# Optimization experiments

Hardware: AMD Instinct MI355X
Metric: run time of the kernel (lower is better)

Reference implementation:

```python
import jax, jax.numpy as jnp
import numpy as np
from jax import lax

B, T, K = 32, 2048, 1024


def setup_inputs() -> dict:
    key = jax.random.key(0)
    x = jax.random.normal(key, (B, T, K), dtype=jnp.float32)
    return {"x": x}


def reference(x) -> jnp.ndarray:
    # x: [B, T, K]. Max-plus DP:
    #   out[:, 0]   = x[:, 0]
    #   out[:, i+1] = x[:, i+1] + max(out[:, i], shift_right(out[:, i], -inf))
    neg_inf = jnp.asarray(-jnp.inf, dtype=x.dtype)
    x_t = jnp.swapaxes(x, 0, 1)  # [T, B, K] time-major for scan

    def step(carry, xi):
        # carry: [B, K] = out row i; xi: [B, K] = x row i+1
        shifted = jnp.concatenate(
            [jnp.full_like(carry[:, :1], neg_inf), carry[:, :-1]], axis=1
        )
        new = xi + jnp.maximum(carry, shifted)
        return new, new

    init = x_t[0]
    _, rows = lax.scan(step, init, x_t[1:])  # rows: [T-1, B, K]
    out = jnp.concatenate([init[None], rows], axis=0)  # [T, B, K]
    return jnp.swapaxes(out, 0, 1)  # [B, T, K]
```

## Files before the change

### kernel.cpp

```cpp
#include <hip/hip_runtime.h>
#include <math.h>


#define BB 32
#define TT 2048
#define KK 1024
#define GG 8
#define WW (KK / GG)
#define RR 32
#define NT (TT / RR)

typedef __attribute__((address_space(1))) void GV;
typedef __attribute__((address_space(3))) void LV;

__global__ __launch_bounds__(64, 1)
void harddtw_td(const float* __restrict__ x, float* __restrict__ out,
                int* __restrict__ flags, float* __restrict__ bws)
{
    const int bid  = blockIdx.x;
    const int g    = bid >> 5;
    const int b    = bid & 31;
    const int lane = threadIdx.x;
    const bool lz  = (lane == 0);

    const int k0 = g * WW;
    const int kc = k0 + (lane << 1);
    const size_t base = (size_t)b * TT * KK;

    float* ol = out + base + kc;

    int* myflag = flags + bid;
    int* upflag = flags + bid - 32;
    float*       mybw = bws + ((size_t)(b * GG + g)) * TT;
    const float* upbw = bws + ((size_t)(b * GG + g - 1)) * TT;

    __shared__ float lds[2][RR * WW];

    const float* xstage = x + base + k0 + (size_t)(lane >> 5) * KK
                          + ((lane & 31) << 2);

    {
        const float* gp = xstage;
#pragma unroll
        for (int i = 0; i < RR / 2; ++i) {
            __builtin_amdgcn_global_load_lds((GV*)(void*)gp,
                                             (LV*)(void*)&lds[0][i * 256],
                                             16, 0, 0);
            gp += 2 * KK;
        }
    }

    float pv0 = 0.0f, pv1 = 0.0f;
    float sh_prev = 0.0f;
    float bcur = -INFINITY, bnxt = -INFINITY;

    if (g > 0) {
        while (__hip_atomic_load(upflag, __ATOMIC_RELAXED,
                                 __HIP_MEMORY_SCOPE_AGENT) < 1)
            __builtin_amdgcn_s_sleep(1);
        __asm__ volatile("" ::: "memory");
        if (lane == 0) {
            bcur = 0.0f;
        } else if (lane < RR) {
            bcur = __hip_atomic_load(upbw + lane - 1, __ATOMIC_RELAXED,
                                     __HIP_MEMORY_SCOPE_AGENT);
        }
    }

    __asm__ volatile("s_waitcnt vmcnt(0)" ::: "memory");

    int buf = 0;

#pragma unroll 1
    for (int r = 0; r < NT; ++r) {
        if (g > 0 && r < NT - 1) {
            while (__hip_atomic_load(upflag, __ATOMIC_RELAXED,
                                     __HIP_MEMORY_SCOPE_AGENT) < r + 2)
                __builtin_amdgcn_s_sleep(1);
            __asm__ volatile("" ::: "memory");
            if (lane < RR)
                bnxt = __hip_atomic_load(
                    upbw + (size_t)(r + 1) * RR + lane - 1,
                    __ATOMIC_RELAXED, __HIP_MEMORY_SCOPE_AGENT);
        }

        if (r < NT - 1) {
            const float* gp = xstage + (size_t)(r + 1) * RR * KK;
            float* lp = &lds[buf ^ 1][0];
#pragma unroll
            for (int i = 0; i < RR / 2; ++i) {
                __builtin_amdgcn_global_load_lds((GV*)(void*)gp,
                                                 (LV*)(void*)(lp + i * 256),
                                                 16, 0, 0);
                gp += 2 * KK;
            }
        }

        float2 td[RR];
#pragma unroll
        for (int j = 0; j < RR; ++j)
            td[j] = *(const float2*)&lds[buf][j * WW + (lane << 1)];
        __builtin_amdgcn_sched_barrier(0);

        const bool pub = (g < GG - 1);
        float bpair = 0.0f;

#pragma unroll
        for (int j = 0; j < RR; ++j) {
            float2 xv = td[j];
            float n1 = xv.y + fmaxf(pv1, pv0);
            float sh_new = __shfl_up(n1, 1);
            float bv = __int_as_float(
                __builtin_amdgcn_readlane(__float_as_int(bcur), j));
            float left = lz ? bv : sh_prev;
            float n0 = xv.x + fmaxf(pv0, left);

            float2 o; o.x = n0; o.y = n1;
            *(float2*)ol = o;
            ol += KK;

            if ((j & 1) == 0) {
                bpair = n1;
            } else if (pub && lane == 63) {
                union { float f[2]; unsigned long long u; } cv;
                cv.f[0] = bpair; cv.f[1] = n1;
                __hip_atomic_store(
                    (unsigned long long*)(mybw + (size_t)r * RR + (j - 1)),
                    cv.u, __ATOMIC_RELAXED, __HIP_MEMORY_SCOPE_AGENT);
            }

            pv0 = n0; pv1 = n1; sh_prev = sh_new;
        }

        bcur = bnxt;

        __asm__ volatile("s_waitcnt vmcnt(0)" ::: "memory");
        if (pub && lz)
            __hip_atomic_store(myflag, r + 1, __ATOMIC_RELAXED,
                               __HIP_MEMORY_SCOPE_AGENT);

        buf ^= 1;
    }
}

extern "C" void kernel_launch(void* const* d_in, const int* in_sizes, int n_in,
                              void* d_out, int out_size, void* d_ws, size_t ws_size,
                              hipStream_t stream) {
    (void)in_sizes; (void)n_in; (void)out_size; (void)ws_size;
    const float* x = (const float*)d_in[0];
    float* out = (float*)d_out;
    int* flags = (int*)d_ws;
    float* bws = (float*)((char*)d_ws + 4096);

    hipMemsetAsync(flags, 0, BB * GG * sizeof(int), stream);

    harddtw_td<<<dim3(BB * GG), dim3(64), 0, stream>>>(x, out, flags, bws);
}
```

Measured before the change: 598.3 us.

## Defer boundary publishing and flag release to overlap cross-block handoff with compute

```diff
diff --git a/kernel.cpp b/kernel.cpp
--- a/kernel.cpp
+++ b/kernel.cpp
@@ -14,7 +14,7 @@
 typedef __attribute__((address_space(3))) void LV;
 
 __global__ __launch_bounds__(64, 1)
-void harddtw_td(const float* __restrict__ x, float* __restrict__ out,
+void harddtw_nd(const float* __restrict__ x, float* __restrict__ out,
                 int* __restrict__ flags, float* __restrict__ bws)
 {
     const int bid  = blockIdx.x;
@@ -53,6 +53,9 @@
     float pv0 = 0.0f, pv1 = 0.0f;
     float sh_prev = 0.0f;
     float bcur = -INFINITY, bnxt = -INFINITY;
+    unsigned long long bp[16];
+#pragma unroll
+    for (int i = 0; i < 16; ++i) bp[i] = 0ull;
 
     if (g > 0) {
         while (__hip_atomic_load(upflag, __ATOMIC_RELAXED,
@@ -68,21 +71,24 @@
     }
 
     __asm__ volatile("s_waitcnt vmcnt(0)" ::: "memory");
-
+    int fpre = 0;
     int buf = 0;
 
 #pragma unroll 1
     for (int r = 0; r < NT; ++r) {
-        if (g > 0 && r < NT - 1) {
-            while (__hip_atomic_load(upflag, __ATOMIC_RELAXED,
-                                     __HIP_MEMORY_SCOPE_AGENT) < r + 2)
-                __builtin_amdgcn_s_sleep(1);
-            __asm__ volatile("" ::: "memory");
-            if (lane < RR)
-                bnxt = __hip_atomic_load(
-                    upbw + (size_t)(r + 1) * RR + lane - 1,
-                    __ATOMIC_RELAXED, __HIP_MEMORY_SCOPE_AGENT);
+        const bool pub = (g < GG - 1);
+
+        __asm__ volatile("s_waitcnt vmcnt(32)" ::: "memory");
+
+        if (pub && r > 0 && lane == 63) {
+            unsigned long long* bwp =
+                (unsigned long long*)(mybw + (size_t)(r - 1) * RR);
+#pragma unroll
+            for (int i = 0; i < 16; ++i)
+                __hip_atomic_store(bwp + i, bp[i], __ATOMIC_RELAXED,
+                                   __HIP_MEMORY_SCOPE_AGENT);
         }
+        __asm__ volatile("" ::: "memory");
 
         if (r < NT - 1) {
             const float* gp = xstage + (size_t)(r + 1) * RR * KK;
@@ -95,6 +101,16 @@
                 gp += 2 * KK;
             }
         }
+        __asm__ volatile("" ::: "memory");
+
+        if (g > 0 && r < NT - 1) {
+            if (fpre < r + 2) {
+                while (__hip_atomic_load(upflag, __ATOMIC_RELAXED,
+                                         __HIP_MEMORY_SCOPE_AGENT) < r + 2)
+                    __builtin_amdgcn_s_sleep(1);
+            }
+            __asm__ volatile("" ::: "memory");
+        }
 
         float2 td[RR];
 #pragma unroll
@@ -102,9 +118,7 @@
             td[j] = *(const float2*)&lds[buf][j * WW + (lane << 1)];
         __builtin_amdgcn_sched_barrier(0);
 
-        const bool pub = (g < GG - 1);
-        float bpair = 0.0f;
-
+        float bpe = 0.0f;
 #pragma unroll
         for (int j = 0; j < RR; ++j) {
             float2 xv = td[j];
@@ -120,26 +134,52 @@
             ol += KK;
 
             if ((j & 1) == 0) {
-                bpair = n1;
-            } else if (pub && lane == 63) {
+                bpe = n1;
+            } else {
                 union { float f[2]; unsigned long long u; } cv;
-                cv.f[0] = bpair; cv.f[1] = n1;
-                __hip_atomic_store(
-                    (unsigned long long*)(mybw + (size_t)r * RR + (j - 1)),
-                    cv.u, __ATOMIC_RELAXED, __HIP_MEMORY_SCOPE_AGENT);
+                cv.f[0] = bpe; cv.f[1] = n1;
+                bp[j >> 1] = cv.u;
             }
 
             pv0 = n0; pv1 = n1; sh_prev = sh_new;
         }
+        __asm__ volatile("" ::: "memory");
 
+        if (g > 0 && r < NT - 1) {
+            if (lane < RR)
+                bnxt = __hip_atomic_load(
+                    upbw + (size_t)(r + 1) * RR + lane - 1,
+                    __ATOMIC_RELAXED, __HIP_MEMORY_SCOPE_AGENT);
+            if (r < NT - 2)
+                fpre = __hip_atomic_load(upflag, __ATOMIC_RELAXED,
+                                         __HIP_MEMORY_SCOPE_AGENT);
+        }
         bcur = bnxt;
+        __asm__ volatile("" ::: "memory");
 
-        __asm__ volatile("s_waitcnt vmcnt(0)" ::: "memory");
-        if (pub && lz)
-            __hip_atomic_store(myflag, r + 1, __ATOMIC_RELAXED,
-                               __HIP_MEMORY_SCOPE_AGENT);
+        if (pub && r > 0) {
+            __asm__ volatile("s_waitcnt vmcnt(48)" ::: "memory");
+            if (lz)
+                __hip_atomic_store(myflag, r, __ATOMIC_RELAXED,
+                                   __HIP_MEMORY_SCOPE_AGENT);
+        }
 
         buf ^= 1;
+    }
+
+    if (g < GG - 1) {
+        if (lane == 63) {
+            unsigned long long* bwp =
+                (unsigned long long*)(mybw + (size_t)(NT - 1) * RR);
+#pragma unroll
+            for (int i = 0; i < 16; ++i)
+                __hip_atomic_store(bwp + i, bp[i], __ATOMIC_RELAXED,
+                                   __HIP_MEMORY_SCOPE_AGENT);
+        }
+        __asm__ volatile("s_waitcnt vmcnt(0)" ::: "memory");
+        if (lz)
+            __hip_atomic_store(myflag, NT, __ATOMIC_RELAXED,
+                               __HIP_MEMORY_SCOPE_AGENT);
     }
 }
 
@@ -154,5 +194,5 @@
 
     hipMemsetAsync(flags, 0, BB * GG * sizeof(int), stream);
 
-    harddtw_td<<<dim3(BB * GG), dim3(64), 0, stream>>>(x, out, flags, bws);
+    harddtw_nd<<<dim3(BB * GG), dim3(64), 0, stream>>>(x, out, flags, bws);
 }
```

After: 593.6 us. No clear change (-0.8%).

## Warp-specialize DP kernel into compute, load, and store wavefronts

Applied to the files above, without the earlier changes.

```diff
diff --git a/kernel.cpp b/kernel.cpp
--- a/kernel.cpp
+++ b/kernel.cpp
@@ -8,138 +8,210 @@
 #define GG 8
 #define WW (KK / GG)
 #define RR 32
+#define HH 16
 #define NT (TT / RR)
 
 typedef __attribute__((address_space(1))) void GV;
 typedef __attribute__((address_space(3))) void LV;
 
-__global__ __launch_bounds__(64, 1)
-void harddtw_td(const float* __restrict__ x, float* __restrict__ out,
+#define BAR() do {                                              \
+    __asm__ volatile("s_waitcnt lgkmcnt(0)" ::: "memory");      \
+    __builtin_amdgcn_s_barrier();                               \
+    __builtin_amdgcn_sched_barrier(0);                          \
+} while (0)
+
+__global__ __launch_bounds__(256, 1)
+void harddtw_ws(const float* __restrict__ x, float* __restrict__ out,
                 int* __restrict__ flags, float* __restrict__ bws)
 {
     const int bid  = blockIdx.x;
     const int g    = bid >> 5;
     const int b    = bid & 31;
-    const int lane = threadIdx.x;
+    const int w    = threadIdx.x >> 6;
+    const int lane = threadIdx.x & 63;
     const bool lz  = (lane == 0);
 
     const int k0 = g * WW;
     const int kc = k0 + (lane << 1);
     const size_t base = (size_t)b * TT * KK;
-
-    float* ol = out + base + kc;
 
     int* myflag = flags + bid;
     int* upflag = flags + bid - 32;
     float*       mybw = bws + ((size_t)(b * GG + g)) * TT;
     const float* upbw = bws + ((size_t)(b * GG + g - 1)) * TT;
 
-    __shared__ float lds[2][RR * WW];
+    __shared__ float xbuf[2][RR * WW];
+    __shared__ float obuf[2][HH * WW];
 
     const float* xstage = x + base + k0 + (size_t)(lane >> 5) * KK
                           + ((lane & 31) << 2);
 
-    {
-        const float* gp = xstage;
-#pragma unroll
-        for (int i = 0; i < RR / 2; ++i) {
-            __builtin_amdgcn_global_load_lds((GV*)(void*)gp,
-                                             (LV*)(void*)&lds[0][i * 256],
-                                             16, 0, 0);
-            gp += 2 * KK;
-        }
-    }
+    const bool pub = (g < GG - 1);
 
     float pv0 = 0.0f, pv1 = 0.0f;
     float sh_prev = 0.0f;
     float bcur = -INFINITY, bnxt = -INFINITY;
-
-    if (g > 0) {
+    int   bndv = 0;
+    int   fpre = 0;
+
+    if (w == 1) {
+        const float* gp = xstage;
+#pragma unroll
+        for (int i = 0; i < RR / 2; ++i) {
+            __builtin_amdgcn_global_load_lds((GV*)(void*)gp,
+                                             (LV*)(void*)&xbuf[0][i * 256],
+                                             16, 0, 0);
+            gp += 2 * KK;
+        }
+        __asm__ volatile("s_waitcnt vmcnt(0)" ::: "memory");
+    }
+    if (w == 0 && g > 0) {
         while (__hip_atomic_load(upflag, __ATOMIC_RELAXED,
                                  __HIP_MEMORY_SCOPE_AGENT) < 1)
             __builtin_amdgcn_s_sleep(1);
         __asm__ volatile("" ::: "memory");
-        if (lane == 0) {
-            bcur = 0.0f;
-        } else if (lane < RR) {
+        if (lz) bcur = 0.0f;
+        else if (lane < RR)
             bcur = __hip_atomic_load(upbw + lane - 1, __ATOMIC_RELAXED,
                                      __HIP_MEMORY_SCOPE_AGENT);
-        }
-    }
-
-    __asm__ volatile("s_waitcnt vmcnt(0)" ::: "memory");
-
-    int buf = 0;
+    }
+    BAR();
 
 #pragma unroll 1
     for (int r = 0; r < NT; ++r) {
-        if (g > 0 && r < NT - 1) {
-            while (__hip_atomic_load(upflag, __ATOMIC_RELAXED,
-                                     __HIP_MEMORY_SCOPE_AGENT) < r + 2)
-                __builtin_amdgcn_s_sleep(1);
-            __asm__ volatile("" ::: "memory");
-            if (lane < RR)
-                bnxt = __hip_atomic_load(
-                    upbw + (size_t)(r + 1) * RR + lane - 1,
-                    __ATOMIC_RELAXED, __HIP_MEMORY_SCOPE_AGENT);
-        }
-
-        if (r < NT - 1) {
-            const float* gp = xstage + (size_t)(r + 1) * RR * KK;
-            float* lp = &lds[buf ^ 1][0];
-#pragma unroll
-            for (int i = 0; i < RR / 2; ++i) {
-                __builtin_amdgcn_global_load_lds((GV*)(void*)gp,
-                                                 (LV*)(void*)(lp + i * 256),
-                                                 16, 0, 0);
-                gp += 2 * KK;
-            }
-        }
-
-        float2 td[RR];
-#pragma unroll
-        for (int j = 0; j < RR; ++j)
-            td[j] = *(const float2*)&lds[buf][j * WW + (lane << 1)];
-        __builtin_amdgcn_sched_barrier(0);
-
-        const bool pub = (g < GG - 1);
-        float bpair = 0.0f;
-
-#pragma unroll
-        for (int j = 0; j < RR; ++j) {
-            float2 xv = td[j];
-            float n1 = xv.y + fmaxf(pv1, pv0);
-            float sh_new = __shfl_up(n1, 1);
-            float bv = __int_as_float(
-                __builtin_amdgcn_readlane(__float_as_int(bcur), j));
-            float left = lz ? bv : sh_prev;
-            float n0 = xv.x + fmaxf(pv0, left);
-
-            float2 o; o.x = n0; o.y = n1;
-            *(float2*)ol = o;
-            ol += KK;
-
-            if ((j & 1) == 0) {
-                bpair = n1;
-            } else if (pub && lane == 63) {
-                union { float f[2]; unsigned long long u; } cv;
-                cv.f[0] = bpair; cv.f[1] = n1;
-                __hip_atomic_store(
-                    (unsigned long long*)(mybw + (size_t)r * RR + (j - 1)),
-                    cv.u, __ATOMIC_RELAXED, __HIP_MEMORY_SCOPE_AGENT);
-            }
-
-            pv0 = n0; pv1 = n1; sh_prev = sh_new;
-        }
-
-        bcur = bnxt;
-
-        __asm__ volatile("s_waitcnt vmcnt(0)" ::: "memory");
-        if (pub && lz)
-            __hip_atomic_store(myflag, r + 1, __ATOMIC_RELAXED,
-                               __HIP_MEMORY_SCOPE_AGENT);
-
-        buf ^= 1;
+        const int cur = r & 1;
+
+        if (w == 0) {
+            float2 td[HH];
+#pragma unroll
+            for (int j = 0; j < HH; ++j)
+                td[j] = *(const float2*)&xbuf[cur][j * WW + (lane << 1)];
+            __builtin_amdgcn_sched_barrier(0);
+            float2 ov[HH];
+#pragma unroll
+            for (int j = 0; j < HH; ++j) {
+                float2 xv = td[j];
+                float n1 = xv.y + fmaxf(pv1, pv0);
+                float sh_new = __shfl_up(n1, 1);
+                float bv = __int_as_float(
+                    __builtin_amdgcn_readlane(__float_as_int(bcur), j));
+                float left = lz ? bv : sh_prev;
+                float n0 = xv.x + fmaxf(pv0, left);
+                ov[j].x = n0; ov[j].y = n1;
+                {
+                    int b63 = __builtin_amdgcn_readlane(__float_as_int(n1), 63);
+                    if (lane == j) bndv = b63;
+                }
+                pv0 = n0; pv1 = n1; sh_prev = sh_new;
+            }
+#pragma unroll
+            for (int j = 0; j < HH; ++j)
+                *(float2*)&obuf[0][j * WW + (lane << 1)] = ov[j];
+        } else if (w >= 2 && r > 0) {
+            const int sw = w - 2;
+            float* ob = out + base
+                      + (size_t)((r - 1) * RR + HH + sw * 8) * KK + kc;
+#pragma unroll
+            for (int i = 0; i < 8; ++i) {
+                float2 v = *(const float2*)&obuf[1][(sw * 8 + i) * WW
+                                                    + (lane << 1)];
+                *(float2*)ob = v;
+                ob += KK;
+            }
+        }
+        BAR();
+
+        if (w == 0) {
+            float2 td[HH];
+#pragma unroll
+            for (int j = 0; j < HH; ++j)
+                td[j] = *(const float2*)&xbuf[cur][(HH + j) * WW + (lane << 1)];
+            __builtin_amdgcn_sched_barrier(0);
+            float2 ov[HH];
+#pragma unroll
+            for (int j = 0; j < HH; ++j) {
+                float2 xv = td[j];
+                float n1 = xv.y + fmaxf(pv1, pv0);
+                float sh_new = __shfl_up(n1, 1);
+                float bv = __int_as_float(
+                    __builtin_amdgcn_readlane(__float_as_int(bcur), HH + j));
+                float left = lz ? bv : sh_prev;
+                float n0 = xv.x + fmaxf(pv0, left);
+                ov[j].x = n0; ov[j].y = n1;
+                {
+                    int b63 = __builtin_amdgcn_readlane(__float_as_int(n1), 63);
+                    if (lane == HH + j) bndv = b63;
+                }
+                pv0 = n0; pv1 = n1; sh_prev = sh_new;
+            }
+#pragma unroll
+            for (int j = 0; j < HH; ++j)
+                *(float2*)&obuf[1][j * WW + (lane << 1)] = ov[j];
+
+            if (pub) {
+                if (lane < RR)
+                    __hip_atomic_store(mybw + (size_t)r * RR + lane,
+                                       __int_as_float(bndv),
+                                       __ATOMIC_RELAXED,
+                                       __HIP_MEMORY_SCOPE_AGENT);
+                __asm__ volatile("s_waitcnt vmcnt(0)" ::: "memory");
+                if (lz)
+                    __hip_atomic_store(myflag, r + 1, __ATOMIC_RELAXED,
+                                       __HIP_MEMORY_SCOPE_AGENT);
+            }
+            if (g > 0 && r < NT - 1) {
+                if (fpre < r + 2) {
+                    while (__hip_atomic_load(upflag, __ATOMIC_RELAXED,
+                                             __HIP_MEMORY_SCOPE_AGENT) < r + 2)
+                        __builtin_amdgcn_s_sleep(1);
+                }
+                __asm__ volatile("" ::: "memory");
+                if (lane < RR)
+                    bnxt = __hip_atomic_load(
+                               upbw + (size_t)(r + 1) * RR + lane - 1,
+                               __ATOMIC_RELAXED, __HIP_MEMORY_SCOPE_AGENT);
+                fpre = __hip_atomic_load(upflag, __ATOMIC_RELAXED,
+                                         __HIP_MEMORY_SCOPE_AGENT);
+            }
+            bcur = bnxt;
+        } else if (w == 1) {
+            if (r < NT - 1) {
+                const float* gp = xstage + (size_t)(r + 1) * RR * KK;
+                float* lp = &xbuf[cur ^ 1][0];
+#pragma unroll
+                for (int i = 0; i < RR / 2; ++i) {
+                    __builtin_amdgcn_global_load_lds((GV*)(void*)gp,
+                                                     (LV*)(void*)(lp + i * 256),
+                                                     16, 0, 0);
+                    gp += 2 * KK;
+                }
+                __asm__ volatile("s_waitcnt vmcnt(0)" ::: "memory");
+            }
+        } else if (w >= 2) {
+            const int sw = w - 2;
+            float* ob = out + base + (size_t)(r * RR + sw * 8) * KK + kc;
+#pragma unroll
+            for (int i = 0; i < 8; ++i) {
+                float2 v = *(const float2*)&obuf[0][(sw * 8 + i) * WW
+                                                    + (lane << 1)];
+                *(float2*)ob = v;
+                ob += KK;
+            }
+        }
+        BAR();
+    }
+
+    if (w >= 2) {
+        const int sw = w - 2;
+        float* ob = out + base
+                  + (size_t)((NT - 1) * RR + HH + sw * 8) * KK + kc;
+#pragma unroll
+        for (int i = 0; i < 8; ++i) {
+            float2 v = *(const float2*)&obuf[1][(sw * 8 + i) * WW
+                                                + (lane << 1)];
+            *(float2*)ob = v;
+            ob += KK;
+        }
     }
 }
 
@@ -152,7 +224,7 @@
     int* flags = (int*)d_ws;
     float* bws = (float*)((char*)d_ws + 4096);
 
-    hipMemsetAsync(flags, 0, BB * GG * sizeof(int), stream);
-
-    harddtw_td<<<dim3(BB * GG), dim3(64), 0, stream>>>(x, out, flags, bws);
+    (void)hipMemsetAsync(flags, 0, BB * GG * sizeof(int), stream);
+
+    harddtw_ws<<<dim3(BB * GG), dim3(256), 0, stream>>>(x, out, flags, bws);
 }
```

Measured after the change: 557.0 us. 6.9% less time.
